# Optimization experiments

Hardware: AMD Instinct MI355X
Metric: run time of the kernel (lower is better)

The kernel has to match this reference:

```python
import jax, jax.numpy as jnp
import numpy as np

GROUP_SIZE = 64
IN_FEATURES = 4096
OUT_FEATURES = 4096
NUM_GROUPS = OUT_FEATURES * IN_FEATURES // GROUP_SIZE  # 262144
BYTES_PER_GROUP = GROUP_SIZE // 8 * 3  # 24
TOKENS = 8192


def block_dequantize_3bit(packed, scale, group_size=GROUP_SIZE):
    # packed: (G, bytes_per_group) int32 holding byte values 0..255
    p = packed.astype(jnp.uint8).astype(jnp.int32)  # byte semantics
    t = p.reshape(p.shape[0], -1, 3)  # (G, group_size//8, 3)
    b0, b1, b2 = t[..., 0], t[..., 1], t[..., 2]
    c0 = b0 & 7
    c1 = (b0 >> 3) & 7
    c2 = ((b0 >> 6) & 3) | ((b1 & 1) << 2)
    c3 = (b1 >> 1) & 7
    c4 = (b1 >> 4) & 7
    c5 = ((b1 >> 7) & 1) | ((b2 & 3) << 1)
    c6 = (b2 >> 2) & 7
    c7 = (b2 >> 5) & 7
    codes = jnp.stack([c0, c1, c2, c3, c4, c5, c6, c7], axis=-1)
    codes = codes.reshape(p.shape[0], group_size)  # (G, group_size)
    q = jnp.clip(codes - 3, -3, 3).astype(jnp.float32)
    return (q * scale.astype(jnp.float32)).reshape(-1)


def setup_inputs() -> dict:
    key = jax.random.key(0)
    k1, k2, k3, k4 = jax.random.split(key, 4)
    x = jax.random.normal(k1, (TOKENS, IN_FEATURES), dtype=jnp.float32)
    weight_q3 = jax.random.randint(k2, (NUM_GROUPS, BYTES_PER_GROUP), 0, 256, dtype=jnp.int32)
    weight_scale = jax.random.uniform(k3, (NUM_GROUPS, 1), dtype=jnp.float32)
    bias = jax.random.normal(k4, (OUT_FEATURES,), dtype=jnp.float32)
    return {"x": x, "weight_q3": weight_q3, "weight_scale": weight_scale, "bias": bias}


def reference(x, weight_q3, weight_scale, bias):
    w = block_dequantize_3bit(weight_q3, weight_scale).reshape(OUT_FEATURES, IN_FEATURES)
    out = jnp.einsum('ti,oi->to', x.astype(jnp.float32), w) + bias
    return out.astype(x.dtype)
```

## Files before the change

### kernel.cpp

```cpp
#include <hip/hip_runtime.h>

#define M_TOK 8192
#define N_OUT 4096
#define K_IN  4096
#define BK    64
#define NT    (K_IN / BK)

typedef __bf16 bf16;
typedef bf16  bf16x4  __attribute__((ext_vector_type(4)));
typedef bf16  bf16x8  __attribute__((ext_vector_type(8)));
typedef float floatx4 __attribute__((ext_vector_type(4)));

__device__ __forceinline__ bf16 dec_code(int c, float s) {
    int q = (c > 6 ? 6 : c) - 3;
    return (bf16)((float)q * s);
}

__device__ __forceinline__ void async_ld16(const bf16* g, const bf16* l) {
    __builtin_amdgcn_global_load_lds(
        (const __attribute__((address_space(1))) void*)g,
        (__attribute__((address_space(3))) void*)l,
        16, 0, 0);
}

__global__ __launch_bounds__(256)
void dequant_kernel(const int* __restrict__ wq, const float* __restrict__ wscale,
                    bf16* __restrict__ W)
{
    int idx  = blockIdx.x * 256 + threadIdx.x;
    int g    = idx >> 1;
    int half = idx & 1;
    const int* wp = wq + (size_t)g * 24 + half * 12;
    int4 r0 = *(const int4*)(wp);
    int4 r1 = *(const int4*)(wp + 4);
    int4 r2 = *(const int4*)(wp + 8);
    float s = wscale[g];
    int by[12] = { r0.x, r0.y, r0.z, r0.w, r1.x, r1.y, r1.z, r1.w,
                   r2.x, r2.y, r2.z, r2.w };
    bf16* dst = W + (size_t)g * 64 + half * 32;
#pragma unroll
    for (int tri = 0; tri < 4; ++tri) {
        int b0 = by[tri * 3 + 0];
        int b1 = by[tri * 3 + 1];
        int b2 = by[tri * 3 + 2];
        bf16x8 h;
        h[0] = dec_code(b0 & 7, s);
        h[1] = dec_code((b0 >> 3) & 7, s);
        h[2] = dec_code(((b0 >> 6) & 3) | ((b1 & 1) << 2), s);
        h[3] = dec_code((b1 >> 1) & 7, s);
        h[4] = dec_code((b1 >> 4) & 7, s);
        h[5] = dec_code(((b1 >> 7) & 1) | ((b2 & 3) << 1), s);
        h[6] = dec_code((b2 >> 2) & 7, s);
        h[7] = dec_code((b2 >> 5) & 7, s);
        *(bf16x8*)(dst + tri * 8) = h;
    }
}

__global__ __launch_bounds__(256)
void cvt_kernel(const float* __restrict__ x, bf16* __restrict__ xb)
{
    size_t i = ((size_t)blockIdx.x * 256 + threadIdx.x) * 8;
    float4 a = *(const float4*)(x + i);
    float4 b = *(const float4*)(x + i + 4);
    bf16x8 h = { (bf16)a.x, (bf16)a.y, (bf16)a.z, (bf16)a.w,
                 (bf16)b.x, (bf16)b.y, (bf16)b.z, (bf16)b.w };
    *(bf16x8*)(xb + i) = h;
}

__global__ __launch_bounds__(256, 2)
void gemm_kernel(const bf16* __restrict__ A, const bf16* __restrict__ B,
                 const float* __restrict__ bias, float* __restrict__ out)
{
    __shared__ bf16 As[2][128][BK];
    __shared__ bf16 Bs[2][128][BK];

    const int t     = threadIdx.x;
    const int nBase = blockIdx.x * 128;
    const int mBase = blockIdx.y * 128;

    const int wave = t >> 6;
    const int lane = t & 63;
    const int quad = lane >> 4;
    const int r16  = lane & 15;
    const int wm   = wave & 1;
    const int wn   = wave >> 1;

    const int wEven = __builtin_amdgcn_readfirstlane(wm) == 0;

    const int rr  = lane >> 3;
    const int cc  = lane & 7;
    const int lch = cc ^ rr;

    const bf16* aBase = A + (size_t)(mBase + wave * 32 + rr) * K_IN + lch * 8;
    const bf16* bBase = B + (size_t)(nBase + wave * 32 + rr) * K_IN + lch * 8;
    const bf16* aLds  = &As[0][wave * 32][0] + lane * 8;
    const bf16* bLds  = &Bs[0][wave * 32][0] + lane * 8;
    const int bufElems = 128 * BK;

    floatx4 acc[4][4];
#pragma unroll
    for (int i = 0; i < 4; ++i)
#pragma unroll
        for (int j = 0; j < 4; ++j)
            acc[i][j] = (floatx4){0.f, 0.f, 0.f, 0.f};

    const int sw = r16 & 7;

#pragma unroll
    for (int j = 0; j < 4; ++j)
        async_ld16(bBase + (size_t)j * 8 * K_IN, bLds + j * 8 * BK);
#pragma unroll
    for (int j = 0; j < 4; ++j)
        async_ld16(aBase + (size_t)j * 8 * K_IN, aLds + j * 8 * BK);

    for (int kt = 0; kt < NT; ++kt) {
        const int  cb   = kt & 1;
        const int  nb   = cb ^ 1;
        const bool haveNext = (kt + 1 < NT);

        if (haveNext) {
#pragma unroll
            for (int j = 0; j < 4; ++j)
                async_ld16(bBase + (size_t)j * 8 * K_IN + (size_t)(kt + 1) * BK,
                           bLds + nb * bufElems + j * 8 * BK);
#pragma unroll
            for (int j = 0; j < 4; ++j)
                async_ld16(aBase + (size_t)j * 8 * K_IN + (size_t)(kt + 1) * BK,
                           aLds + nb * bufElems + j * 8 * BK);
        }

        if (haveNext) {
            if (wEven) asm volatile("s_waitcnt vmcnt(8)\n\ts_barrier" ::: "memory");
            else       asm volatile("s_waitcnt vmcnt(12)\n\ts_barrier" ::: "memory");
        } else {
            if (wEven) asm volatile("s_waitcnt vmcnt(0)\n\ts_barrier" ::: "memory");
            else       asm volatile("s_waitcnt vmcnt(4)\n\ts_barrier" ::: "memory");
        }

        bf16x8 bfr[2][4], afA[2][2];
#pragma unroll
        for (int ks = 0; ks < 2; ++ks) {
#pragma unroll
            for (int ni = 0; ni < 4; ++ni)
                bfr[ks][ni] = *(const bf16x8*)(&Bs[cb][wn * 64 + ni * 16 + r16]
                                                 [((ks * 4 + quad) ^ sw) * 8]);
#pragma unroll
            for (int mi = 0; mi < 2; ++mi)
                afA[ks][mi] = *(const bf16x8*)(&As[cb][wm * 64 + mi * 16 + r16]
                                                 [((ks * 4 + quad) ^ sw) * 8]);
        }
        __builtin_amdgcn_s_setprio(1);
#pragma unroll
        for (int ks = 0; ks < 2; ++ks)
#pragma unroll
            for (int mi = 0; mi < 2; ++mi)
#pragma unroll
                for (int ni = 0; ni < 4; ++ni)
                    acc[mi][ni] = __builtin_amdgcn_mfma_f32_16x16x32_bf16(
                        afA[ks][mi], bfr[ks][ni], acc[mi][ni], 0, 0, 0);
        __builtin_amdgcn_s_setprio(0);

        if (wEven) {
            asm volatile("s_barrier" ::: "memory");
        } else if (haveNext) {
            asm volatile("s_waitcnt vmcnt(8)\n\ts_barrier" ::: "memory");
        } else {
            asm volatile("s_waitcnt vmcnt(0)\n\ts_barrier" ::: "memory");
        }

        bf16x8 afB[2][2];
#pragma unroll
        for (int ks = 0; ks < 2; ++ks)
#pragma unroll
            for (int mi = 0; mi < 2; ++mi)
                afB[ks][mi] = *(const bf16x8*)(&As[cb][wm * 64 + (mi + 2) * 16 + r16]
                                                 [((ks * 4 + quad) ^ sw) * 8]);
        __builtin_amdgcn_s_setprio(1);
#pragma unroll
        for (int ks = 0; ks < 2; ++ks)
#pragma unroll
            for (int mi = 0; mi < 2; ++mi)
#pragma unroll
                for (int ni = 0; ni < 4; ++ni)
                    acc[mi + 2][ni] = __builtin_amdgcn_mfma_f32_16x16x32_bf16(
                        afB[ks][mi], bfr[ks][ni], acc[mi + 2][ni], 0, 0, 0);
        __builtin_amdgcn_s_setprio(0);

        if (haveNext) asm volatile("s_barrier" ::: "memory");
    }

    const int colBase = nBase + wn * 64;
#pragma unroll
    for (int ni = 0; ni < 4; ++ni) {
        int col  = colBase + ni * 16 + r16;
        float bv = bias[col];
#pragma unroll
        for (int mi = 0; mi < 4; ++mi) {
            int row0 = mBase + wm * 64 + mi * 16 + quad * 4;
#pragma unroll
            for (int r = 0; r < 4; ++r)
                out[(size_t)(row0 + r) * N_OUT + col] = acc[mi][ni][r] + bv;
        }
    }
}

__global__ __launch_bounds__(256, 2)
void linear3bit_fused(const float* __restrict__ x,
                      const int*   __restrict__ wq,
                      const float* __restrict__ wscale,
                      const float* __restrict__ bias,
                      float*       __restrict__ out)
{
    __shared__ bf16 As[128][BK];
    __shared__ bf16 Bs[128][BK];

    const int t     = threadIdx.x;
    const int mBase = blockIdx.y * 128;
    const int nBase = blockIdx.x * 128;

    const int wave = t >> 6;
    const int lane = t & 63;
    const int quad = lane >> 4;
    const int r16  = lane & 15;
    const int wm   = wave & 1;
    const int wn   = wave >> 1;

    floatx4 acc[4][4];
#pragma unroll
    for (int i = 0; i < 4; ++i)
#pragma unroll
        for (int j = 0; j < 4; ++j)
            acc[i][j] = (floatx4){0.f, 0.f, 0.f, 0.f};

    const int gl   = t >> 1;
    const int half = t & 1;
    const float* xBase = x + (size_t)mBase * K_IN;

    float4 aReg[8];
    int4   bReg[3];
    float  sReg;

    auto loadTile = [&](int kt) {
#pragma unroll
        for (int i = 0; i < 8; ++i) {
            int linear = i * 256 + t;
            int row    = linear >> 4;
            int c4     = (linear & 15) << 2;
            aReg[i] = *(const float4*)(xBase + (size_t)row * K_IN + kt * BK + c4);
        }
        size_t g = (size_t)(nBase + gl) * 64 + kt;
        const int* wp = wq + g * 24 + half * 12;
        bReg[0] = *(const int4*)(wp);
        bReg[1] = *(const int4*)(wp + 4);
        bReg[2] = *(const int4*)(wp + 8);
        sReg = wscale[g];
    };

    auto stage = [&]() {
#pragma unroll
        for (int i = 0; i < 8; ++i) {
            int linear = i * 256 + t;
            int row    = linear >> 4;
            int c4     = (linear & 15) << 2;
            float4 v = aReg[i];
            bf16x4 h = { (bf16)v.x, (bf16)v.y, (bf16)v.z, (bf16)v.w };
            *(bf16x4*)(&As[row][c4]) = h;
        }
        const float s = sReg;
        int by[12] = { bReg[0].x, bReg[0].y, bReg[0].z, bReg[0].w,
                       bReg[1].x, bReg[1].y, bReg[1].z, bReg[1].w,
                       bReg[2].x, bReg[2].y, bReg[2].z, bReg[2].w };
#pragma unroll
        for (int tri = 0; tri < 4; ++tri) {
            int b0 = by[tri * 3 + 0];
            int b1 = by[tri * 3 + 1];
            int b2 = by[tri * 3 + 2];
            bf16x8 h;
            h[0] = dec_code(b0 & 7, s);
            h[1] = dec_code((b0 >> 3) & 7, s);
            h[2] = dec_code(((b0 >> 6) & 3) | ((b1 & 1) << 2), s);
            h[3] = dec_code((b1 >> 1) & 7, s);
            h[4] = dec_code((b1 >> 4) & 7, s);
            h[5] = dec_code(((b1 >> 7) & 1) | ((b2 & 3) << 1), s);
            h[6] = dec_code((b2 >> 2) & 7, s);
            h[7] = dec_code((b2 >> 5) & 7, s);
            *(bf16x8*)(&Bs[gl][half * 32 + tri * 8]) = h;
        }
    };

    auto compute = [&]() {
#pragma unroll
        for (int ks = 0; ks < 2; ++ks) {
            bf16x8 af[4], bfr[4];
#pragma unroll
            for (int mi = 0; mi < 4; ++mi)
                af[mi] = *(const bf16x8*)(&As[wm * 64 + mi * 16 + r16][ks * 32 + quad * 8]);
#pragma unroll
            for (int ni = 0; ni < 4; ++ni)
                bfr[ni] = *(const bf16x8*)(&Bs[wn * 64 + ni * 16 + r16][ks * 32 + quad * 8]);
#pragma unroll
            for (int mi = 0; mi < 4; ++mi)
#pragma unroll
                for (int ni = 0; ni < 4; ++ni)
                    acc[mi][ni] = __builtin_amdgcn_mfma_f32_16x16x32_bf16(
                        af[mi], bfr[ni], acc[mi][ni], 0, 0, 0);
        }
    };

    loadTile(0);
    for (int kt = 0; kt < NT; ++kt) {
        __syncthreads();
        stage();
        __syncthreads();
        if (kt + 1 < NT) loadTile(kt + 1);
        compute();
    }

    const int colBase = nBase + wn * 64;
#pragma unroll
    for (int ni = 0; ni < 4; ++ni) {
        int col  = colBase + ni * 16 + r16;
        float bv = bias[col];
#pragma unroll
        for (int mi = 0; mi < 4; ++mi) {
            int row0 = mBase + wm * 64 + mi * 16 + quad * 4;
#pragma unroll
            for (int r = 0; r < 4; ++r)
                out[(size_t)(row0 + r) * N_OUT + col] = acc[mi][ni][r] + bv;
        }
    }
}

extern "C" void kernel_launch(void* const* d_in, const int* in_sizes, int n_in,
                              void* d_out, int out_size, void* d_ws, size_t ws_size,
                              hipStream_t stream) {
    const float* x      = (const float*)d_in[0];
    const int*   wq     = (const int*)d_in[1];
    const float* wscale = (const float*)d_in[2];
    const float* bias   = (const float*)d_in[3];
    float*       out    = (float*)d_out;

    const size_t wBytes  = (size_t)N_OUT * K_IN * sizeof(bf16);
    const size_t xBytes  = (size_t)M_TOK * K_IN * sizeof(bf16);

    if (ws_size >= wBytes + xBytes) {
        bf16* Wb = (bf16*)d_ws;
        bf16* Xb = (bf16*)((char*)d_ws + wBytes);
        dequant_kernel<<<2048, 256, 0, stream>>>(wq, wscale, Wb);
        cvt_kernel<<<16384, 256, 0, stream>>>(x, Xb);
        dim3 grid(N_OUT / 128, M_TOK / 128);
        gemm_kernel<<<grid, dim3(256), 0, stream>>>(Xb, Wb, bias, out);
    } else {
        dim3 grid(N_OUT / 128, M_TOK / 128);
        linear3bit_fused<<<grid, dim3(256), 0, stream>>>(x, wq, wscale, bias, out);
    }
}
```

Measured before the change: 512.4 us.

## Enlarge GEMM tile to 256x256 with 8 waves and merge prep kernels

The GEMM moves from 128x128 tiles with 4 waves to 256x256 tiles with 8 waves (each wave computing 128x64). Loads for the next k-tile are interleaved between MFMA groups under a new waitcnt/barrier schedule. The dequant and fp32->bf16 conversion kernels are merged into one launch. The larger tile cuts global/L2 traffic per flop, but uses 128KB of LDS and limits occupancy to one block per CU.

New measurement: 538.4 us. 5.1% more time.

```diff
diff --git a/kernel.cpp b/kernel.cpp
--- a/kernel.cpp
+++ b/kernel.cpp
@@ -24,170 +24,154 @@
 }
 
 __global__ __launch_bounds__(256)
-void dequant_kernel(const int* __restrict__ wq, const float* __restrict__ wscale,
-                    bf16* __restrict__ W)
+void prep_kernel(const int* __restrict__ wq, const float* __restrict__ wscale,
+                 const float* __restrict__ x,
+                 bf16* __restrict__ W, bf16* __restrict__ xb)
 {
-    int idx  = blockIdx.x * 256 + threadIdx.x;
-    int g    = idx >> 1;
-    int half = idx & 1;
-    const int* wp = wq + (size_t)g * 24 + half * 12;
-    int4 r0 = *(const int4*)(wp);
-    int4 r1 = *(const int4*)(wp + 4);
-    int4 r2 = *(const int4*)(wp + 8);
-    float s = wscale[g];
-    int by[12] = { r0.x, r0.y, r0.z, r0.w, r1.x, r1.y, r1.z, r1.w,
-                   r2.x, r2.y, r2.z, r2.w };
-    bf16* dst = W + (size_t)g * 64 + half * 32;
-#pragma unroll
-    for (int tri = 0; tri < 4; ++tri) {
-        int b0 = by[tri * 3 + 0];
-        int b1 = by[tri * 3 + 1];
-        int b2 = by[tri * 3 + 2];
-        bf16x8 h;
-        h[0] = dec_code(b0 & 7, s);
-        h[1] = dec_code((b0 >> 3) & 7, s);
-        h[2] = dec_code(((b0 >> 6) & 3) | ((b1 & 1) << 2), s);
-        h[3] = dec_code((b1 >> 1) & 7, s);
-        h[4] = dec_code((b1 >> 4) & 7, s);
-        h[5] = dec_code(((b1 >> 7) & 1) | ((b2 & 3) << 1), s);
-        h[6] = dec_code((b2 >> 2) & 7, s);
-        h[7] = dec_code((b2 >> 5) & 7, s);
-        *(bf16x8*)(dst + tri * 8) = h;
-    }
-}
-
-__global__ __launch_bounds__(256)
-void cvt_kernel(const float* __restrict__ x, bf16* __restrict__ xb)
-{
-    size_t i = ((size_t)blockIdx.x * 256 + threadIdx.x) * 8;
-    float4 a = *(const float4*)(x + i);
-    float4 b = *(const float4*)(x + i + 4);
-    bf16x8 h = { (bf16)a.x, (bf16)a.y, (bf16)a.z, (bf16)a.w,
-                 (bf16)b.x, (bf16)b.y, (bf16)b.z, (bf16)b.w };
-    *(bf16x8*)(xb + i) = h;
-}
-
-__global__ __launch_bounds__(256, 2)
+    const int b = blockIdx.x;
+    const int t = threadIdx.x;
+    if (b < 2048) {
+        int idx  = b * 256 + t;
+        int g    = idx >> 1;
+        int half = idx & 1;
+        const int* wp = wq + (size_t)g * 24 + half * 12;
+        int4 r0 = *(const int4*)(wp);
+        int4 r1 = *(const int4*)(wp + 4);
+        int4 r2 = *(const int4*)(wp + 8);
+        float s = wscale[g];
+        int by[12] = { r0.x, r0.y, r0.z, r0.w, r1.x, r1.y, r1.z, r1.w,
+                       r2.x, r2.y, r2.z, r2.w };
+        bf16* dst = W + (size_t)g * 64 + half * 32;
+#pragma unroll
+        for (int tri = 0; tri < 4; ++tri) {
+            int b0 = by[tri * 3 + 0];
+            int b1 = by[tri * 3 + 1];
+            int b2 = by[tri * 3 + 2];
+            bf16x8 h;
+            h[0] = dec_code(b0 & 7, s);
+            h[1] = dec_code((b0 >> 3) & 7, s);
+            h[2] = dec_code(((b0 >> 6) & 3) | ((b1 & 1) << 2), s);
+            h[3] = dec_code((b1 >> 1) & 7, s);
+            h[4] = dec_code((b1 >> 4) & 7, s);
+            h[5] = dec_code(((b1 >> 7) & 1) | ((b2 & 3) << 1), s);
+            h[6] = dec_code((b2 >> 2) & 7, s);
+            h[7] = dec_code((b2 >> 5) & 7, s);
+            *(bf16x8*)(dst + tri * 8) = h;
+        }
+    } else {
+        size_t i = ((size_t)(b - 2048) * 256 + t) * 8;
+        float4 a = *(const float4*)(x + i);
+        float4 c = *(const float4*)(x + i + 4);
+        bf16x8 h = { (bf16)a.x, (bf16)a.y, (bf16)a.z, (bf16)a.w,
+                     (bf16)c.x, (bf16)c.y, (bf16)c.z, (bf16)c.w };
+        *(bf16x8*)(xb + i) = h;
+    }
+}
+
+__global__ __launch_bounds__(512, 2)
 void gemm_kernel(const bf16* __restrict__ A, const bf16* __restrict__ B,
                  const float* __restrict__ bias, float* __restrict__ out)
 {
-    __shared__ bf16 As[2][128][BK];
-    __shared__ bf16 Bs[2][128][BK];
+    __shared__ bf16 As[2][256][BK];
+    __shared__ bf16 Bs[2][256][BK];
 
     const int t     = threadIdx.x;
-    const int nBase = blockIdx.x * 128;
-    const int mBase = blockIdx.y * 128;
+    const int nBase = blockIdx.x * 256;
+    const int mBase = blockIdx.y * 256;
 
     const int wave = t >> 6;
     const int lane = t & 63;
     const int quad = lane >> 4;
     const int r16  = lane & 15;
-    const int wm   = wave & 1;
-    const int wn   = wave >> 1;
-
-    const int wEven = __builtin_amdgcn_readfirstlane(wm) == 0;
-
-    const int rr  = lane >> 3;
-    const int cc  = lane & 7;
-    const int lch = cc ^ rr;
-
-    const bf16* aBase = A + (size_t)(mBase + wave * 32 + rr) * K_IN + lch * 8;
-    const bf16* bBase = B + (size_t)(nBase + wave * 32 + rr) * K_IN + lch * 8;
-    const bf16* aLds  = &As[0][wave * 32][0] + lane * 8;
-    const bf16* bLds  = &Bs[0][wave * 32][0] + lane * 8;
-    const int bufElems = 128 * BK;
-
-    floatx4 acc[4][4];
-#pragma unroll
-    for (int i = 0; i < 4; ++i)
+    const int wm   = wave >> 2;
+    const int wn   = wave & 3;
+    const int sw   = r16 & 7;
+
+    const int rowInBlk = t >> 3;
+    const int lc       = (t & 7) ^ (rowInBlk & 7);
+
+    const bf16* aSrc = A + (size_t)(mBase + rowInBlk) * K_IN + lc * 8;
+    const bf16* bSrc = B + (size_t)(nBase + rowInBlk) * K_IN + lc * 8;
+    bf16* aLds0 = &As[0][0][0] + t * 8;
+    bf16* bLds0 = &Bs[0][0][0] + t * 8;
+
+#define STAGE_A(KT1, BUF, ROFF) \
+    async_ld16(aSrc + (size_t)(ROFF) * K_IN + (size_t)(KT1) * BK, \
+               aLds0 + (BUF) * 16384 + (ROFF) * BK)
+#define STAGE_B(KT1, BUF, ROFF) \
+    async_ld16(bSrc + (size_t)(ROFF) * K_IN + (size_t)(KT1) * BK, \
+               bLds0 + (BUF) * 16384 + (ROFF) * BK)
+
+    floatx4 acc[8][4];
+#pragma unroll
+    for (int i = 0; i < 8; ++i)
 #pragma unroll
         for (int j = 0; j < 4; ++j)
             acc[i][j] = (floatx4){0.f, 0.f, 0.f, 0.f};
 
-    const int sw = r16 & 7;
-
-#pragma unroll
-    for (int j = 0; j < 4; ++j)
-        async_ld16(bBase + (size_t)j * 8 * K_IN, bLds + j * 8 * BK);
-#pragma unroll
-    for (int j = 0; j < 4; ++j)
-        async_ld16(aBase + (size_t)j * 8 * K_IN, aLds + j * 8 * BK);
+    STAGE_B(0, 0, 0);   STAGE_B(0, 0, 64);  STAGE_B(0, 0, 128); STAGE_B(0, 0, 192);
+    STAGE_A(0, 0, 0);   STAGE_A(0, 0, 128); STAGE_A(0, 0, 64);  STAGE_A(0, 0, 192);
+
+    bf16x8 bfr[2][4];
+
+#define MFMA_PAIR(CB, M0) do {                                                  \
+        bf16x8 af_[2][2];                                                       \
+        _Pragma("unroll")                                                       \
+        for (int ks = 0; ks < 2; ++ks)                                          \
+            _Pragma("unroll")                                                   \
+            for (int q = 0; q < 2; ++q)                                         \
+                af_[ks][q] = *(const bf16x8*)(&As[CB][wm * 128 + ((M0) + q) * 16 + r16] \
+                                                 [((ks * 4 + quad) ^ sw) * 8]); \
+        __builtin_amdgcn_s_setprio(1);                                          \
+        _Pragma("unroll")                                                       \
+        for (int ks = 0; ks < 2; ++ks)                                          \
+            _Pragma("unroll")                                                   \
+            for (int q = 0; q < 2; ++q)                                         \
+                _Pragma("unroll")                                               \
+                for (int ni = 0; ni < 4; ++ni)                                  \
+                    acc[(M0) + q][ni] = __builtin_amdgcn_mfma_f32_16x16x32_bf16(\
+                        af_[ks][q], bfr[ks][ni], acc[(M0) + q][ni], 0, 0, 0);   \
+        __builtin_amdgcn_s_setprio(0);                                          \
+    } while (0)
 
     for (int kt = 0; kt < NT; ++kt) {
-        const int  cb   = kt & 1;
-        const int  nb   = cb ^ 1;
-        const bool haveNext = (kt + 1 < NT);
-
-        if (haveNext) {
-#pragma unroll
-            for (int j = 0; j < 4; ++j)
-                async_ld16(bBase + (size_t)j * 8 * K_IN + (size_t)(kt + 1) * BK,
-                           bLds + nb * bufElems + j * 8 * BK);
-#pragma unroll
-            for (int j = 0; j < 4; ++j)
-                async_ld16(aBase + (size_t)j * 8 * K_IN + (size_t)(kt + 1) * BK,
-                           aLds + nb * bufElems + j * 8 * BK);
-        }
-
-        if (haveNext) {
-            if (wEven) asm volatile("s_waitcnt vmcnt(8)\n\ts_barrier" ::: "memory");
-            else       asm volatile("s_waitcnt vmcnt(12)\n\ts_barrier" ::: "memory");
-        } else {
-            if (wEven) asm volatile("s_waitcnt vmcnt(0)\n\ts_barrier" ::: "memory");
-            else       asm volatile("s_waitcnt vmcnt(4)\n\ts_barrier" ::: "memory");
-        }
-
-        bf16x8 bfr[2][4], afA[2][2];
-#pragma unroll
-        for (int ks = 0; ks < 2; ++ks) {
+        const int  cb = kt & 1;
+        const int  nb = cb ^ 1;
+        const bool hn = (kt + 1 < NT);
+
+        asm volatile("s_waitcnt vmcnt(2)\n\ts_barrier" ::: "memory");
+
+        if (hn) {
+            STAGE_B(kt + 1, nb, 0);   STAGE_B(kt + 1, nb, 64);
+            STAGE_B(kt + 1, nb, 128); STAGE_B(kt + 1, nb, 192);
+        }
+
+#pragma unroll
+        for (int ks = 0; ks < 2; ++ks)
 #pragma unroll
             for (int ni = 0; ni < 4; ++ni)
                 bfr[ks][ni] = *(const bf16x8*)(&Bs[cb][wn * 64 + ni * 16 + r16]
-                                                 [((ks * 4 + quad) ^ sw) * 8]);
-#pragma unroll
-            for (int mi = 0; mi < 2; ++mi)
-                afA[ks][mi] = *(const bf16x8*)(&As[cb][wm * 64 + mi * 16 + r16]
-                                                 [((ks * 4 + quad) ^ sw) * 8]);
-        }
-        __builtin_amdgcn_s_setprio(1);
-#pragma unroll
-        for (int ks = 0; ks < 2; ++ks)
-#pragma unroll
-            for (int mi = 0; mi < 2; ++mi)
-#pragma unroll
-                for (int ni = 0; ni < 4; ++ni)
-                    acc[mi][ni] = __builtin_amdgcn_mfma_f32_16x16x32_bf16(
-                        afA[ks][mi], bfr[ks][ni], acc[mi][ni], 0, 0, 0);
-        __builtin_amdgcn_s_setprio(0);
-
-        if (wEven) {
-            asm volatile("s_barrier" ::: "memory");
-        } else if (haveNext) {
-            asm volatile("s_waitcnt vmcnt(8)\n\ts_barrier" ::: "memory");
-        } else {
-            asm volatile("s_waitcnt vmcnt(0)\n\ts_barrier" ::: "memory");
-        }
-
-        bf16x8 afB[2][2];
-#pragma unroll
-        for (int ks = 0; ks < 2; ++ks)
-#pragma unroll
-            for (int mi = 0; mi < 2; ++mi)
-                afB[ks][mi] = *(const bf16x8*)(&As[cb][wm * 64 + (mi + 2) * 16 + r16]
-                                                 [((ks * 4 + quad) ^ sw) * 8]);
-        __builtin_amdgcn_s_setprio(1);
-#pragma unroll
-        for (int ks = 0; ks < 2; ++ks)
-#pragma unroll
-            for (int mi = 0; mi < 2; ++mi)
-#pragma unroll
-                for (int ni = 0; ni < 4; ++ni)
-                    acc[mi + 2][ni] = __builtin_amdgcn_mfma_f32_16x16x32_bf16(
-                        afB[ks][mi], bfr[ks][ni], acc[mi + 2][ni], 0, 0, 0);
-        __builtin_amdgcn_s_setprio(0);
-
-        if (haveNext) asm volatile("s_barrier" ::: "memory");
-    }
+                                                  [((ks * 4 + quad) ^ sw) * 8]);
+
+        MFMA_PAIR(cb, 0);
+
+        if (hn) {
+            STAGE_A(kt + 1, nb, 0);  STAGE_A(kt + 1, nb, 128);
+            STAGE_A(kt + 1, nb, 64); STAGE_A(kt + 1, nb, 192);
+        }
+
+        MFMA_PAIR(cb, 2);
+
+        if (hn) asm volatile("s_waitcnt vmcnt(8)\n\ts_barrier" ::: "memory");
+        else    asm volatile("s_waitcnt vmcnt(0)\n\ts_barrier" ::: "memory");
+
+        MFMA_PAIR(cb, 4);
+        MFMA_PAIR(cb, 6);
+    }
+
+#undef MFMA_PAIR
+#undef STAGE_A
+#undef STAGE_B
 
     const int colBase = nBase + wn * 64;
 #pragma unroll
@@ -195,8 +179,8 @@
         int col  = colBase + ni * 16 + r16;
         float bv = bias[col];
 #pragma unroll
-        for (int mi = 0; mi < 4; ++mi) {
-            int row0 = mBase + wm * 64 + mi * 16 + quad * 4;
+        for (int mi = 0; mi < 8; ++mi) {
+            int row0 = mBase + wm * 128 + mi * 16 + quad * 4;
 #pragma unroll
             for (int r = 0; r < 4; ++r)
                 out[(size_t)(row0 + r) * N_OUT + col] = acc[mi][ni][r] + bv;
@@ -346,10 +330,9 @@
     if (ws_size >= wBytes + xBytes) {
         bf16* Wb = (bf16*)d_ws;
         bf16* Xb = (bf16*)((char*)d_ws + wBytes);
-        dequant_kernel<<<2048, 256, 0, stream>>>(wq, wscale, Wb);
-        cvt_kernel<<<16384, 256, 0, stream>>>(x, Xb);
-        dim3 grid(N_OUT / 128, M_TOK / 128);
-        gemm_kernel<<<grid, dim3(256), 0, stream>>>(Xb, Wb, bias, out);
+        prep_kernel<<<2048 + 16384, 256, 0, stream>>>(wq, wscale, x, Wb, Xb);
+        dim3 grid(N_OUT / 256, M_TOK / 256);
+        gemm_kernel<<<grid, dim3(512), 0, stream>>>(Xb, Wb, bias, out);
     } else {
         dim3 grid(N_OUT / 128, M_TOK / 128);
         linear3bit_fused<<<grid, dim3(256), 0, stream>>>(x, wq, wscale, bias, out);
```
